# Optimization experiments

Measured on AMD Instinct MI355X. Metric: run time of the kernel, lower is better.

The kernel has to match this reference:

```python
import jax, jax.numpy as jnp
import numpy as np

B, T = 512, 512
NQ, K, M, DK, DV, DF = 1000, 5, 50, 64, 256, 50
ABILITY_SCALE = 3.0


def setup_inputs() -> dict:
    key = jax.random.key(0)
    ks = jax.random.split(key, 16)
    s = 0.05
    p = {}
    p["q_data"] = jax.random.randint(ks[0], (B, T), 0, NQ + 1)
    p["r_data"] = jax.random.randint(ks[1], (B, T), 0, K)
    p["q_embed_W"] = jax.random.normal(ks[2], (NQ + 1, DK)) * s
    p["Mk"] = jax.random.normal(ks[3], (M, DK)) * s
    p["Mv0"] = jax.random.normal(ks[4], (M, DV)) * s
    p["value_W"] = jax.random.normal(ks[5], (2 * NQ, DV)) * s
    p["value_b"] = jnp.zeros((DV,))
    p["erase_W"] = jax.random.normal(ks[6], (DV, DV)) * s
    p["erase_b"] = jnp.zeros((DV,))
    p["add_W"] = jax.random.normal(ks[7], (DV, DV)) * s
    p["add_b"] = jnp.zeros((DV,))
    p["summary_W"] = jax.random.normal(ks[8], (DV + DK, DF)) * s
    p["summary_b"] = jnp.zeros((DF,))
    p["ability_W"] = jax.random.normal(ks[9], (DF, 1)) * s
    p["ability_b"] = jnp.zeros((1,))
    p["thresh_W"] = jax.random.normal(ks[10], (DK, K - 1)) * s
    p["thresh_b"] = jnp.zeros((K - 1,))
    p["disc_W"] = jax.random.normal(ks[11], (DF + DK, 1)) * s
    p["disc_b"] = jnp.zeros((1,))
    p["corn_W"] = jax.random.normal(ks[12], (DF + DK, K - 1)) * s
    p["corn_b"] = jnp.zeros((K - 1,))
    return p


def reference(q_data, r_data, q_embed_W, Mk, Mv0, value_W, value_b, erase_W, erase_b,
              add_W, add_b, summary_W, summary_b, ability_W, ability_b,
              thresh_W, thresh_b, disc_W, disc_b, corn_W, corn_b):
    nq = value_W.shape[0] // 2
    k_cats = corn_W.shape[1] + 1
    b = q_data.shape[0]
    qe = q_embed_W[q_data]                                # [B,T,DK] question key embedding
    valid = (q_data > 0)[..., None]                       # q==0 is padding (one-hot col dropped)
    idx = jnp.maximum(q_data - 1, 0)
    # ordered embedding [one_hot(q), (r/(K-1))*one_hot(q)] @ value_W == exact row gather
    rs = r_data.astype(qe.dtype) / (k_cats - 1)
    ve = value_W[idx] + rs[..., None] * value_W[nq + idx]
    ve = jnp.where(valid, ve, 0.0) + value_b              # [B,T,DV]
    # attention over key memory (time-independent, hoisted out of the recurrence)
    w = jax.nn.softmax(jnp.einsum('btk,mk->btm', qe, Mk), axis=-1)  # [B,T,M]
    erase = jax.nn.sigmoid(ve @ erase_W + erase_b)        # [B,T,DV]
    add = jnp.tanh(ve @ add_W + add_b)                    # [B,T,DV]
    Mv_init = jnp.broadcast_to(Mv0, (b,) + Mv0.shape)     # [B,M,DV]

    def step(Mv, inp):
        w_t, e_t, a_t = inp                               # [B,M], [B,DV], [B,DV]
        read = jnp.einsum('bm,bmv->bv', w_t, Mv)          # read BEFORE write (t reads state < t)
        Mv = Mv * (1.0 - w_t[:, :, None] * e_t[:, None, :]) + w_t[:, :, None] * a_t[:, None, :]
        return Mv, read

    _, reads = jax.lax.scan(step, Mv_init,
                            (jnp.swapaxes(w, 0, 1), jnp.swapaxes(erase, 0, 1), jnp.swapaxes(add, 0, 1)))
    reads = jnp.swapaxes(reads, 0, 1)                     # [B,T,DV]

    summary = jnp.tanh(jnp.concatenate([reads, qe], -1) @ summary_W + summary_b)  # [B,T,DF]
    theta = (summary @ ability_W + ability_b)[..., 0] * ABILITY_SCALE             # [B,T]
    betas = qe @ thresh_W + thresh_b                                              # [B,T,K-1]
    di = jnp.concatenate([summary, qe], -1)                                       # [B,T,DF+DK]
    alpha = jax.nn.softplus(di @ disc_W + disc_b)[..., 0]                         # [B,T]
    logits = di @ corn_W + corn_b                                                 # [B,T,K-1]
    # CORN: cumulative conditional probs -> class probabilities
    cp = jnp.cumprod(jax.nn.sigmoid(logits), axis=-1)     # P(y > k)
    upper = jnp.concatenate([jnp.ones_like(cp[..., :1]), cp], -1)
    lower = jnp.concatenate([cp, jnp.zeros_like(cp[..., :1])], -1)
    probs = upper - lower                                 # [B,T,K]
    return theta, betas, alpha, probs, logits
```

## Files before the change

### kernel.cpp

```cpp
#include <hip/hip_runtime.h>

typedef unsigned short u16;
typedef unsigned int u32;
typedef __bf16 bf16x8 __attribute__((ext_vector_type(8)));
typedef float fx4 __attribute__((ext_vector_type(4)));
typedef float fx2 __attribute__((ext_vector_type(2)));

#define NT 262144
#define B_SZ 512
#define T_LEN 512
#define NQv 1000
#define LP 40
#define VE_ROWS 5120

__device__ __forceinline__ float bf2f(u16 u) { return __uint_as_float(((u32)u) << 16); }
__device__ __forceinline__ u16 f2bf(float f) {
    u32 x = __float_as_uint(f);
    x += 0x7fffu + ((x >> 16) & 1u);
    return (u16)(x >> 16);
}
__device__ __forceinline__ u32 pack2(float a, float b) {
    return (u32)f2bf(a) | ((u32)f2bf(b) << 16);
}
__device__ __forceinline__ float sigm(float x) { return 1.0f / (1.0f + __expf(-x)); }
__device__ __forceinline__ float tanh_fast(float x) {
    float e2 = __expf(2.0f * x);
    return 1.0f - 2.0f / (e2 + 1.0f);
}
__device__ __forceinline__ void load_lds16(const void* g, void* l) {
    __builtin_amdgcn_global_load_lds(
        (const __attribute__((address_space(1))) u32*)g,
        (__attribute__((address_space(3))) u32*)l, 16, 0, 0);
}

__global__ __launch_bounds__(256) void k_prep_w(const float* __restrict__ eW,
                                                const float* __restrict__ aW,
                                                const float* __restrict__ sW,
                                                u16* __restrict__ Wt,
                                                u16* __restrict__ SWt) {
    int id = blockIdx.x * 256 + threadIdx.x;
    if (id < 131072) {
        int n = id >> 8, k = id & 255;
        Wt[n * 256 + k] = f2bf((n < 256) ? eW[k * 256 + n] : aW[k * 256 + (n - 256)]);
    } else {
        int id2 = id - 131072;
        if (id2 < 64 * 320) {
            int n = id2 / 320, k = id2 - n * 320;
            SWt[n * 320 + k] = (n < 50) ? f2bf(sW[k * 50 + n]) : (u16)0;
        }
    }
}

__global__ __launch_bounds__(256) void k_w_tab(const float* __restrict__ qeW,
                                               const float* __restrict__ Mk,
                                               float* __restrict__ w_tab) {
    __shared__ __align__(16) float mk[3200];
    int tid = threadIdx.x;
    for (int i = tid; i < 3200; i += 256) mk[i] = Mk[i];
    int q = blockIdx.x * 256 + tid;
    __syncthreads();
    if (q > NQv) return;

    float qe[64];
    {
        const float4* qr = (const float4*)(qeW + (size_t)q * 64);
#pragma unroll
        for (int i = 0; i < 16; i++) {
            float4 u = qr[i];
            qe[4 * i + 0] = u.x; qe[4 * i + 1] = u.y;
            qe[4 * i + 2] = u.z; qe[4 * i + 3] = u.w;
        }
    }
    float lg[50];
#pragma unroll
    for (int m = 0; m < 50; m++) {
        const float* mr = &mk[m * 64];
        float acc = 0.f;
#pragma unroll
        for (int k = 0; k < 64; k++) acc = fmaf(qe[k], mr[k], acc);
        lg[m] = acc;
    }
    float mx = -1e30f;
#pragma unroll
    for (int m = 0; m < 50; m++) mx = fmaxf(mx, lg[m]);
    float sum = 0.f;
#pragma unroll
    for (int m = 0; m < 50; m++) { lg[m] = __expf(lg[m] - mx); sum += lg[m]; }
    float inv = 1.0f / sum;
#pragma unroll
    for (int m = 0; m < 50; m++) w_tab[(size_t)q * 50 + m] = lg[m] * inv;
}

__global__ __launch_bounds__(256) void k_ve_tab(const float* __restrict__ vW,
                                                const float* __restrict__ vb,
                                                u16* __restrict__ ve_tab) {
    int id = blockIdx.x * 256 + threadIdx.x;
    int row = id >> 5, seg = id & 31;
    if (row >= VE_ROWS) return;
    int q = row / 5;
    int r = row - q * 5;
    if (q > NQv) q = NQv;
    int idx = (q > 0) ? (q - 1) : 0;
    float rs = (float)r * 0.25f;
    float vf = (q > 0) ? 1.0f : 0.0f;

    const float* pa = vW + (size_t)idx * 256 + seg * 8;
    const float* pb = pa + NQv * 256;
    float4 a0 = ((const float4*)pa)[0];
    float4 a1 = ((const float4*)pa)[1];
    float4 b0 = ((const float4*)pb)[0];
    float4 b1 = ((const float4*)pb)[1];
    const float* vbp = vb + seg * 8;
    float o0 = vf * fmaf(rs, b0.x, a0.x) + vbp[0];
    float o1 = vf * fmaf(rs, b0.y, a0.y) + vbp[1];
    float o2 = vf * fmaf(rs, b0.z, a0.z) + vbp[2];
    float o3 = vf * fmaf(rs, b0.w, a0.w) + vbp[3];
    float o4 = vf * fmaf(rs, b1.x, a1.x) + vbp[4];
    float o5 = vf * fmaf(rs, b1.y, a1.y) + vbp[5];
    float o6 = vf * fmaf(rs, b1.z, a1.z) + vbp[6];
    float o7 = vf * fmaf(rs, b1.w, a1.w) + vbp[7];
    uint4 o;
    o.x = pack2(o0, o1); o.y = pack2(o2, o3);
    o.z = pack2(o4, o5); o.w = pack2(o6, o7);
    *(uint4*)(ve_tab + (size_t)row * 256 + seg * 8) = o;
}

__global__ __launch_bounds__(256) void k_gemm_ea(const u16* __restrict__ ve,
                                                 const u16* __restrict__ Wt,
                                                 const float* __restrict__ eb,
                                                 const float* __restrict__ ab,
                                                 u16* __restrict__ e_out,
                                                 u16* __restrict__ a_out) {
    __shared__ __align__(16) u16 smem[8192];
    u16* lA = smem;
    u16* lB = smem + 4096;

    int tid = threadIdx.x;
    int row0 = blockIdx.x * 128;
    int col0 = blockIdx.y * 128;

    int wave = tid >> 6, lane = tid & 63;
    int wm = wave >> 1, wn = wave & 1;
    int rl = lane & 15, quad = lane >> 4;
    fx4 acc[4][4] = {};

    int c0 = tid, c1 = tid + 256;
    int r0_ = c0 >> 2, j0 = c0 & 3;
    int r1_ = c1 >> 2, j1 = c1 & 3;

    for (int k0 = 0; k0 < 256; k0 += 32) {
        load_lds16(ve + (size_t)(row0 + r0_) * 256 + k0 + j0 * 8, lA + c0 * 8);
        load_lds16(ve + (size_t)(row0 + r1_) * 256 + k0 + j1 * 8, lA + c1 * 8);
        load_lds16(Wt + (size_t)(col0 + r0_) * 256 + k0 + j0 * 8, lB + c0 * 8);
        load_lds16(Wt + (size_t)(col0 + r1_) * 256 + k0 + j1 * 8, lB + c1 * 8);
        __syncthreads();
        bf16x8 af[4], bfr[4];
#pragma unroll
        for (int i = 0; i < 4; i++) af[i] = *(const bf16x8*)(lA + (wm * 64 + i * 16 + rl) * 32 + quad * 8);
#pragma unroll
        for (int j = 0; j < 4; j++) bfr[j] = *(const bf16x8*)(lB + (wn * 64 + j * 16 + rl) * 32 + quad * 8);
#pragma unroll
        for (int i = 0; i < 4; i++)
#pragma unroll
            for (int j = 0; j < 4; j++)
                acc[i][j] = __builtin_amdgcn_mfma_f32_16x16x32_bf16(af[i], bfr[j], acc[i][j], 0, 0, 0);
        __syncthreads();
    }

    bool is_er = (col0 < 256);
    const float* bias = is_er ? eb : ab;
    u16* outp = is_er ? e_out : a_out;
    int cb0 = col0 & 255;
    u16* cst = smem;
#pragma unroll
    for (int h = 0; h < 2; h++) {
        if (wm == h) {
#pragma unroll
            for (int j = 0; j < 4; j++) {
                int nl = wn * 64 + j * 16 + rl;
                float bv = bias[cb0 + nl];
#pragma unroll
                for (int i = 0; i < 4; i++) {
                    int rowl = i * 16 + quad * 4;
#pragma unroll
                    for (int r = 0; r < 4; r++) {
                        float x = acc[i][j][r] + bv;
                        cst[(rowl + r) * 128 + nl] = f2bf(is_er ? sigm(x) : tanh_fast(x));
                    }
                }
            }
        }
        __syncthreads();
#pragma unroll
        for (int c = 0; c < 4; c++) {
            int idx = c * 256 + tid;
            int row = idx >> 4, seg = idx & 15;
            *(uint4*)(outp + (size_t)(row0 + h * 64 + row) * 256 + cb0 + seg * 8) =
                *(const uint4*)(cst + row * 128 + seg * 8);
        }
        __syncthreads();
    }
}

__global__ __launch_bounds__(256) void k_scan(const int* __restrict__ q_data,
                                              const int* __restrict__ r_data,
                                              const float* __restrict__ w_tab,
                                              const u16* __restrict__ e_tab,
                                              const u16* __restrict__ a_tab,
                                              const float* __restrict__ Mv0,
                                              u16* __restrict__ reads_out) {
    int b = blockIdx.x;
    int tid = threadIdx.x;
    __shared__ float wls[2][8][52];

    const int* qp = q_data + (size_t)b * T_LEN;
    const int* rp = r_data + (size_t)b * T_LEN;

    fx2 Mv[25];
#pragma unroll
    for (int i = 0; i < 25; i++) {
        Mv[i].x = Mv0[(2 * i) * 256 + tid];
        Mv[i].y = Mv0[(2 * i + 1) * 256 + tid];
    }

    u16 eu[8], au[8];
#pragma unroll
    for (int s = 0; s < 8; s++) {
        int qr = qp[s] * 5 + rp[s];
        eu[s] = e_tab[(size_t)qr * 256 + tid];
        au[s] = a_tab[(size_t)qr * 256 + tid];
    }
    if (tid < 200) {
        int s = tid / 25, m2 = tid % 25;
        float2 w0 = ((const float2*)(w_tab + (size_t)qp[s] * 50))[m2];
        wls[0][s][2 * m2] = w0.x;
        wls[0][s][2 * m2 + 1] = w0.y;
    }
    __syncthreads();

    const int ngrp = T_LEN / 8;
    for (int g = 0; g < ngrp; g++) {
        int cur = g & 1, nxt = cur ^ 1;
        bool has_next = (g + 1 < ngrp);
        int tn0 = (g + 1) * 8;

        u16 eun[8], aun[8];
        float2 wn_ = make_float2(0.f, 0.f);
        if (has_next) {
#pragma unroll
            for (int s = 0; s < 8; s++) {
                int qr = qp[tn0 + s] * 5 + rp[tn0 + s];
                eun[s] = e_tab[(size_t)qr * 256 + tid];
                aun[s] = a_tab[(size_t)qr * 256 + tid];
            }
            if (tid < 200) {
                int s = tid / 25, m2 = tid % 25;
                wn_ = ((const float2*)(w_tab + (size_t)qp[tn0 + s] * 50))[m2];
            }
        }

#pragma unroll
        for (int s = 0; s < 8; s++) {
            float e = bf2f(eu[s]), a = bf2f(au[s]);
            fx2 e2; e2.x = e; e2.y = e;
            fx2 a2; a2.x = a; a2.y = a;
            const fx2* wv = (const fx2*)&wls[cur][s][0];
            fx2 rd2; rd2.x = 0.f; rd2.y = 0.f;
#pragma unroll
            for (int i = 0; i < 25; i++) {
                fx2 w2 = wv[i];
                rd2 = rd2 + w2 * Mv[i];
                fx2 t2 = a2 - e2 * Mv[i];
                Mv[i] = Mv[i] + w2 * t2;
            }
            float rd = rd2.x + rd2.y;
            reads_out[((size_t)b * T_LEN + g * 8 + s) * 256 + tid] = f2bf(rd);
        }

        if (has_next) {
            if (tid < 200) {
                int s = tid / 25, m2 = tid % 25;
                wls[nxt][s][2 * m2] = wn_.x;
                wls[nxt][s][2 * m2 + 1] = wn_.y;
            }
#pragma unroll
            for (int s = 0; s < 8; s++) { eu[s] = eun[s]; au[s] = aun[s]; }
        }
        __syncthreads();
    }
}

__global__ __launch_bounds__(256) void k_sum_heads(const u16* __restrict__ reads,
                                                   const int* __restrict__ q_data,
                                                   const float* __restrict__ qeW,
                                                   const u16* __restrict__ SWt,
                                                   const float* __restrict__ sb,
                                                   const float* __restrict__ abilW,
                                                   const float* __restrict__ abilb,
                                                   const float* __restrict__ tW,
                                                   const float* __restrict__ tb,
                                                   const float* __restrict__ dW,
                                                   const float* __restrict__ db,
                                                   const float* __restrict__ cW,
                                                   const float* __restrict__ cb,
                                                   float* __restrict__ out,
                                                   int t0, int tcl2) {
    __shared__ __align__(16) u16 lA[128 * LP];
    __shared__ __align__(16) u16 lB[64 * LP];
    __shared__ float sS[128 * 52];
    __shared__ int s_q[128];
    int tid = threadIdx.x;
    int row0 = blockIdx.x * 128;
    if (tid < 128) {
        int ctok = row0 + tid;
        int b = ctok >> tcl2;
        int tc = ctok & ((1 << tcl2) - 1);
        s_q[tid] = q_data[(b << 9) + t0 + tc];
    }
    int wave = tid >> 6, lane = tid & 63;
    int wm = wave >> 1, wn = wave & 1;
    int rl = lane & 15, quad = lane >> 4;
    fx4 acc[4][2] = {};
    __syncthreads();

    for (int ks = 0; ks < 10; ks++) {
        int k0 = ks * 32;
#pragma unroll
        for (int h = 0; h < 2; h++) {
            int c = tid + h * 256;
            int row = c >> 2, j = c & 3;
            if (k0 < 256) {
                uint4 u = *(const uint4*)(reads + (size_t)(row0 + row) * 256 + k0 + j * 8);
                *(uint4*)(lA + row * LP + j * 8) = u;
            } else {
                const float* src = qeW + (size_t)s_q[row] * 64 + (k0 - 256) + j * 8;
                float4 f0 = ((const float4*)src)[0];
                float4 f1 = ((const float4*)src)[1];
                uint4 o;
                o.x = pack2(f0.x, f0.y); o.y = pack2(f0.z, f0.w);
                o.z = pack2(f1.x, f1.y); o.w = pack2(f1.z, f1.w);
                *(uint4*)(lA + row * LP + j * 8) = o;
            }
        }
        {
            int n = tid >> 2, j = tid & 3;
            uint4 u = *(const uint4*)(SWt + (size_t)n * 320 + k0 + j * 8);
            *(uint4*)(lB + n * LP + j * 8) = u;
        }
        __syncthreads();
        bf16x8 af[4], bfr[2];
#pragma unroll
        for (int i = 0; i < 4; i++) af[i] = *(const bf16x8*)(lA + (wm * 64 + i * 16 + rl) * LP + quad * 8);
#pragma unroll
        for (int j = 0; j < 2; j++) bfr[j] = *(const bf16x8*)(lB + (wn * 32 + j * 16 + rl) * LP + quad * 8);
#pragma unroll
        for (int i = 0; i < 4; i++)
#pragma unroll
            for (int j = 0; j < 2; j++)
                acc[i][j] = __builtin_amdgcn_mfma_f32_16x16x32_bf16(af[i], bfr[j], acc[i][j], 0, 0, 0);
        __syncthreads();
    }

#pragma unroll
    for (int j = 0; j < 2; j++) {
        int n = wn * 32 + j * 16 + rl;
        if (n < 50) {
            float bv = sb[n];
#pragma unroll
            for (int i = 0; i < 4; i++) {
                int rowl = wm * 64 + i * 16 + quad * 4;
#pragma unroll
                for (int r = 0; r < 4; r++)
                    sS[(rowl + r) * 52 + n] = tanh_fast(acc[i][j][r] + bv);
            }
        }
    }
    __syncthreads();

    if (tid < 128) {
        int ctok = row0 + tid;
        int b = ctok >> tcl2;
        int tc = ctok & ((1 << tcl2) - 1);
        int gtok = (b << 9) + t0 + tc;
        const float* sp = &sS[tid * 52];

        float qe[64];
        const float4* qr = (const float4*)(qeW + (size_t)s_q[tid] * 64);
#pragma unroll
        for (int i = 0; i < 16; i++) {
            float4 u = qr[i];
            qe[4 * i + 0] = u.x; qe[4 * i + 1] = u.y;
            qe[4 * i + 2] = u.z; qe[4 * i + 3] = u.w;
        }
        float th = abilb[0];
#pragma unroll
        for (int j = 0; j < 50; j++) th = fmaf(sp[j], abilW[j], th);
        out[gtok] = th * 3.0f;

        float bt0 = tb[0], bt1 = tb[1], bt2 = tb[2], bt3 = tb[3];
#pragma unroll
        for (int k = 0; k < 64; k++) {
            float x = qe[k];
            bt0 = fmaf(x, tW[k * 4 + 0], bt0);
            bt1 = fmaf(x, tW[k * 4 + 1], bt1);
            bt2 = fmaf(x, tW[k * 4 + 2], bt2);
            bt3 = fmaf(x, tW[k * 4 + 3], bt3);
        }
        out[NT + (size_t)gtok * 4 + 0] = bt0;
        out[NT + (size_t)gtok * 4 + 1] = bt1;
        out[NT + (size_t)gtok * 4 + 2] = bt2;
        out[NT + (size_t)gtok * 4 + 3] = bt3;

        float da = db[0];
        float l0 = cb[0], l1 = cb[1], l2 = cb[2], l3 = cb[3];
#pragma unroll
        for (int i = 0; i < 50; i++) {
            float x = sp[i];
            da = fmaf(x, dW[i], da);
            l0 = fmaf(x, cW[i * 4 + 0], l0);
            l1 = fmaf(x, cW[i * 4 + 1], l1);
            l2 = fmaf(x, cW[i * 4 + 2], l2);
            l3 = fmaf(x, cW[i * 4 + 3], l3);
        }
#pragma unroll
        for (int k = 0; k < 64; k++) {
            float x = qe[k];
            int i = 50 + k;
            da = fmaf(x, dW[i], da);
            l0 = fmaf(x, cW[i * 4 + 0], l0);
            l1 = fmaf(x, cW[i * 4 + 1], l1);
            l2 = fmaf(x, cW[i * 4 + 2], l2);
            l3 = fmaf(x, cW[i * 4 + 3], l3);
        }
        float alpha = logf(1.0f + __expf(da));
        out[5 * (size_t)NT + gtok] = alpha;

        out[11 * (size_t)NT + (size_t)gtok * 4 + 0] = l0;
        out[11 * (size_t)NT + (size_t)gtok * 4 + 1] = l1;
        out[11 * (size_t)NT + (size_t)gtok * 4 + 2] = l2;
        out[11 * (size_t)NT + (size_t)gtok * 4 + 3] = l3;

        float c0 = sigm(l0);
        float c1 = c0 * sigm(l1);
        float c2 = c1 * sigm(l2);
        float c3 = c2 * sigm(l3);
        size_t pb = 6 * (size_t)NT + (size_t)gtok * 5;
        out[pb + 0] = 1.0f - c0;
        out[pb + 1] = c0 - c1;
        out[pb + 2] = c1 - c2;
        out[pb + 3] = c2 - c3;
        out[pb + 4] = c3;
    }
}

extern "C" void kernel_launch(void* const* d_in, const int* in_sizes, int n_in,
                              void* d_out, int out_size, void* d_ws, size_t ws_size,
                              hipStream_t stream) {
    (void)in_sizes; (void)n_in; (void)out_size; (void)ws_size;
    const int* q_data = (const int*)d_in[0];
    const int* r_data = (const int*)d_in[1];
    const float* qeW = (const float*)d_in[2];
    const float* Mk  = (const float*)d_in[3];
    const float* Mv0 = (const float*)d_in[4];
    const float* vW  = (const float*)d_in[5];
    const float* vb  = (const float*)d_in[6];
    const float* eW  = (const float*)d_in[7];
    const float* eb  = (const float*)d_in[8];
    const float* aW  = (const float*)d_in[9];
    const float* ab  = (const float*)d_in[10];
    const float* sW  = (const float*)d_in[11];
    const float* sb  = (const float*)d_in[12];
    const float* abilW = (const float*)d_in[13];
    const float* abilb = (const float*)d_in[14];
    const float* tW  = (const float*)d_in[15];
    const float* tb  = (const float*)d_in[16];
    const float* dW  = (const float*)d_in[17];
    const float* db  = (const float*)d_in[18];
    const float* cW  = (const float*)d_in[19];
    const float* cb  = (const float*)d_in[20];

    char* ws = (char*)d_ws;
    u16* Wt     = (u16*)(ws + 0);
    u16* SWt    = (u16*)(ws + 262144);
    float* w_tab = (float*)(ws + 303104);
    u16* ve_tab = (u16*)(ws + 507904);
    u16* e_tab  = (u16*)(ws + 3129344);
    u16* a_tab  = (u16*)(ws + 5750784);
    u16* reads  = (u16*)(ws + 8372224);
    float* out = (float*)d_out;

    k_prep_w<<<592, 256, 0, stream>>>(eW, aW, sW, Wt, SWt);
    k_w_tab<<<4, 256, 0, stream>>>(qeW, Mk, w_tab);
    k_ve_tab<<<VE_ROWS / 8, 256, 0, stream>>>(vW, vb, ve_tab);
    dim3 g2(VE_ROWS / 128, 4);
    k_gemm_ea<<<g2, 256, 0, stream>>>(ve_tab, Wt, eb, ab, e_tab, a_tab);
    k_scan<<<B_SZ, 256, 0, stream>>>(q_data, r_data, w_tab, e_tab, a_tab, Mv0, reads);
    k_sum_heads<<<NT / 128, 256, 0, stream>>>(reads, q_data, qeW, SWt, sb,
                                              abilW, abilb, tW, tb, dW, db, cW, cb,
                                              out, 0, 9);
}
```

Before: 457.5 us.

## Fuse summary GEMM and heads into scan kernel, precompute per-question tables

The scan kernel now keeps each 128-token block of reads in LDS and, every 16 groups, runs the summary MFMA GEMM over the read part plus the per-token heads inline, so the reads buffer is never written to or read back from global memory. The question-embedding contributions (summary qe part, betas, disc and corn qe parts) are precomputed into per-question tables by a new small kernel and then gathered per token. This removes the separate k_sum_heads launch and the reads round trip. In exchange the scan kernel uses much more LDS (about 66 KB), which may cut occupancy, and the serial scan now stalls periodically for the GEMM and head work.

```diff
diff --git a/kernel.cpp b/kernel.cpp
--- a/kernel.cpp
+++ b/kernel.cpp
@@ -10,8 +10,9 @@
 #define B_SZ 512
 #define T_LEN 512
 #define NQv 1000
-#define LP 40
 #define VE_ROWS 5120
+#define TLP 264
+#define SSP 53
 
 __device__ __forceinline__ float bf2f(u16 u) { return __uint_as_float(((u32)u) << 16); }
 __device__ __forceinline__ u16 f2bf(float f) {
@@ -44,9 +45,9 @@
         Wt[n * 256 + k] = f2bf((n < 256) ? eW[k * 256 + n] : aW[k * 256 + (n - 256)]);
     } else {
         int id2 = id - 131072;
-        if (id2 < 64 * 320) {
-            int n = id2 / 320, k = id2 - n * 320;
-            SWt[n * 320 + k] = (n < 50) ? f2bf(sW[k * 50 + n]) : (u16)0;
+        if (id2 < 16384) {
+            int n = id2 >> 8, k = id2 & 255;
+            SWt[n * 256 + k] = (n < 50) ? f2bf(sW[k * 50 + n]) : (u16)0;
         }
     }
 }
@@ -125,6 +126,52 @@
     *(uint4*)(ve_tab + (size_t)row * 256 + seg * 8) = o;
 }
 
+__global__ __launch_bounds__(256) void k_q_tabs(const float* __restrict__ qeW,
+                                                const float* __restrict__ sW,
+                                                const float* __restrict__ tW,
+                                                const float* __restrict__ tb,
+                                                const float* __restrict__ dW,
+                                                const float* __restrict__ cW,
+                                                float* __restrict__ sq_tab,
+                                                float* __restrict__ beta_tab,
+                                                float* __restrict__ dq_tab,
+                                                float* __restrict__ cq_tab) {
+    int id = blockIdx.x * 256 + threadIdx.x;
+    int q = id >> 6, n = id & 63;
+    if (q > NQv) return;
+    float qe[64];
+    const float4* qr = (const float4*)(qeW + (size_t)q * 64);
+#pragma unroll
+    for (int i = 0; i < 16; i++) {
+        float4 u = qr[i];
+        qe[4 * i + 0] = u.x; qe[4 * i + 1] = u.y;
+        qe[4 * i + 2] = u.z; qe[4 * i + 3] = u.w;
+    }
+    if (n < 50) {
+        float acc = 0.f;
+#pragma unroll
+        for (int k = 0; k < 64; k++) acc = fmaf(qe[k], sW[(256 + k) * 50 + n], acc);
+        sq_tab[(size_t)q * 50 + n] = acc;
+    } else if (n < 54) {
+        int j = n - 50;
+        float acc = tb[j];
+#pragma unroll
+        for (int k = 0; k < 64; k++) acc = fmaf(qe[k], tW[k * 4 + j], acc);
+        beta_tab[(size_t)q * 4 + j] = acc;
+    } else if (n == 54) {
+        float acc = 0.f;
+#pragma unroll
+        for (int k = 0; k < 64; k++) acc = fmaf(qe[k], dW[50 + k], acc);
+        dq_tab[q] = acc;
+    } else if (n >= 56 && n < 60) {
+        int j = n - 56;
+        float acc = 0.f;
+#pragma unroll
+        for (int k = 0; k < 64; k++) acc = fmaf(qe[k], cW[(50 + k) * 4 + j], acc);
+        cq_tab[(size_t)q * 4 + j] = acc;
+    }
+}
+
 __global__ __launch_bounds__(256) void k_gemm_ea(const u16* __restrict__ ve,
                                                  const u16* __restrict__ Wt,
                                                  const float* __restrict__ eb,
@@ -202,19 +249,37 @@
     }
 }
 
-__global__ __launch_bounds__(256) void k_scan(const int* __restrict__ q_data,
-                                              const int* __restrict__ r_data,
-                                              const float* __restrict__ w_tab,
-                                              const u16* __restrict__ e_tab,
-                                              const u16* __restrict__ a_tab,
-                                              const float* __restrict__ Mv0,
-                                              u16* __restrict__ reads_out) {
+__global__ __launch_bounds__(256) void k_fused(const int* __restrict__ q_data,
+                                               const int* __restrict__ r_data,
+                                               const float* __restrict__ w_tab,
+                                               const u16* __restrict__ e_tab,
+                                               const u16* __restrict__ a_tab,
+                                               const float* __restrict__ Mv0,
+                                               const u16* __restrict__ SWt,
+                                               const float* __restrict__ sq_tab,
+                                               const float* __restrict__ sb,
+                                               const float* __restrict__ abilW,
+                                               const float* __restrict__ abilb,
+                                               const float* __restrict__ beta_tab,
+                                               const float* __restrict__ dW,
+                                               const float* __restrict__ db,
+                                               const float* __restrict__ dq_tab,
+                                               const float* __restrict__ cW,
+                                               const float* __restrict__ cb,
+                                               const float* __restrict__ cq_tab,
+                                               float* __restrict__ out) {
     int b = blockIdx.x;
     int tid = threadIdx.x;
+    __shared__ __align__(16) u16 tileA[128 * TLP];
     __shared__ float wls[2][8][52];
+    __shared__ int sq_idx[128];
 
     const int* qp = q_data + (size_t)b * T_LEN;
     const int* rp = r_data + (size_t)b * T_LEN;
+
+    int wave = tid >> 6, lane = tid & 63;
+    int wm = wave >> 1, wn = wave & 1;
+    int rl = lane & 15, quad = lane >> 4;
 
     fx2 Mv[25];
 #pragma unroll
@@ -273,8 +338,8 @@
                 fx2 t2 = a2 - e2 * Mv[i];
                 Mv[i] = Mv[i] + w2 * t2;
             }
-            float rd = rd2.x + rd2.y;
-            reads_out[((size_t)b * T_LEN + g * 8 + s) * 256 + tid] = f2bf(rd);
+            int tokrow = (g * 8 + s) & 127;
+            tileA[tokrow * TLP + tid] = f2bf(rd2.x + rd2.y);
         }
 
         if (has_next) {
@@ -287,169 +352,98 @@
             for (int s = 0; s < 8; s++) { eu[s] = eun[s]; au[s] = aun[s]; }
         }
         __syncthreads();
-    }
-}
-
-__global__ __launch_bounds__(256) void k_sum_heads(const u16* __restrict__ reads,
-                                                   const int* __restrict__ q_data,
-                                                   const float* __restrict__ qeW,
-                                                   const u16* __restrict__ SWt,
-                                                   const float* __restrict__ sb,
-                                                   const float* __restrict__ abilW,
-                                                   const float* __restrict__ abilb,
-                                                   const float* __restrict__ tW,
-                                                   const float* __restrict__ tb,
-                                                   const float* __restrict__ dW,
-                                                   const float* __restrict__ db,
-                                                   const float* __restrict__ cW,
-                                                   const float* __restrict__ cb,
-                                                   float* __restrict__ out,
-                                                   int t0, int tcl2) {
-    __shared__ __align__(16) u16 lA[128 * LP];
-    __shared__ __align__(16) u16 lB[64 * LP];
-    __shared__ float sS[128 * 52];
-    __shared__ int s_q[128];
-    int tid = threadIdx.x;
-    int row0 = blockIdx.x * 128;
-    if (tid < 128) {
-        int ctok = row0 + tid;
-        int b = ctok >> tcl2;
-        int tc = ctok & ((1 << tcl2) - 1);
-        s_q[tid] = q_data[(b << 9) + t0 + tc];
-    }
-    int wave = tid >> 6, lane = tid & 63;
-    int wm = wave >> 1, wn = wave & 1;
-    int rl = lane & 15, quad = lane >> 4;
-    fx4 acc[4][2] = {};
-    __syncthreads();
-
-    for (int ks = 0; ks < 10; ks++) {
-        int k0 = ks * 32;
-#pragma unroll
-        for (int h = 0; h < 2; h++) {
-            int c = tid + h * 256;
-            int row = c >> 2, j = c & 3;
-            if (k0 < 256) {
-                uint4 u = *(const uint4*)(reads + (size_t)(row0 + row) * 256 + k0 + j * 8);
-                *(uint4*)(lA + row * LP + j * 8) = u;
-            } else {
-                const float* src = qeW + (size_t)s_q[row] * 64 + (k0 - 256) + j * 8;
-                float4 f0 = ((const float4*)src)[0];
-                float4 f1 = ((const float4*)src)[1];
-                uint4 o;
-                o.x = pack2(f0.x, f0.y); o.y = pack2(f0.z, f0.w);
-                o.z = pack2(f1.x, f1.y); o.w = pack2(f1.z, f1.w);
-                *(uint4*)(lA + row * LP + j * 8) = o;
-            }
-        }
-        {
-            int n = tid >> 2, j = tid & 3;
-            uint4 u = *(const uint4*)(SWt + (size_t)n * 320 + k0 + j * 8);
-            *(uint4*)(lB + n * LP + j * 8) = u;
-        }
-        __syncthreads();
-        bf16x8 af[4], bfr[2];
-#pragma unroll
-        for (int i = 0; i < 4; i++) af[i] = *(const bf16x8*)(lA + (wm * 64 + i * 16 + rl) * LP + quad * 8);
-#pragma unroll
-        for (int j = 0; j < 2; j++) bfr[j] = *(const bf16x8*)(lB + (wn * 32 + j * 16 + rl) * LP + quad * 8);
-#pragma unroll
-        for (int i = 0; i < 4; i++)
-#pragma unroll
-            for (int j = 0; j < 2; j++)
-                acc[i][j] = __builtin_amdgcn_mfma_f32_16x16x32_bf16(af[i], bfr[j], acc[i][j], 0, 0, 0);
-        __syncthreads();
-    }
-
-#pragma unroll
-    for (int j = 0; j < 2; j++) {
-        int n = wn * 32 + j * 16 + rl;
-        if (n < 50) {
-            float bv = sb[n];
-#pragma unroll
-            for (int i = 0; i < 4; i++) {
-                int rowl = wm * 64 + i * 16 + quad * 4;
-#pragma unroll
-                for (int r = 0; r < 4; r++)
-                    sS[(rowl + r) * 52 + n] = tanh_fast(acc[i][j][r] + bv);
-            }
-        }
-    }
-    __syncthreads();
-
-    if (tid < 128) {
-        int ctok = row0 + tid;
-        int b = ctok >> tcl2;
-        int tc = ctok & ((1 << tcl2) - 1);
-        int gtok = (b << 9) + t0 + tc;
-        const float* sp = &sS[tid * 52];
-
-        float qe[64];
-        const float4* qr = (const float4*)(qeW + (size_t)s_q[tid] * 64);
-#pragma unroll
-        for (int i = 0; i < 16; i++) {
-            float4 u = qr[i];
-            qe[4 * i + 0] = u.x; qe[4 * i + 1] = u.y;
-            qe[4 * i + 2] = u.z; qe[4 * i + 3] = u.w;
-        }
-        float th = abilb[0];
-#pragma unroll
-        for (int j = 0; j < 50; j++) th = fmaf(sp[j], abilW[j], th);
-        out[gtok] = th * 3.0f;
-
-        float bt0 = tb[0], bt1 = tb[1], bt2 = tb[2], bt3 = tb[3];
-#pragma unroll
-        for (int k = 0; k < 64; k++) {
-            float x = qe[k];
-            bt0 = fmaf(x, tW[k * 4 + 0], bt0);
-            bt1 = fmaf(x, tW[k * 4 + 1], bt1);
-            bt2 = fmaf(x, tW[k * 4 + 2], bt2);
-            bt3 = fmaf(x, tW[k * 4 + 3], bt3);
-        }
-        out[NT + (size_t)gtok * 4 + 0] = bt0;
-        out[NT + (size_t)gtok * 4 + 1] = bt1;
-        out[NT + (size_t)gtok * 4 + 2] = bt2;
-        out[NT + (size_t)gtok * 4 + 3] = bt3;
-
-        float da = db[0];
-        float l0 = cb[0], l1 = cb[1], l2 = cb[2], l3 = cb[3];
-#pragma unroll
-        for (int i = 0; i < 50; i++) {
-            float x = sp[i];
-            da = fmaf(x, dW[i], da);
-            l0 = fmaf(x, cW[i * 4 + 0], l0);
-            l1 = fmaf(x, cW[i * 4 + 1], l1);
-            l2 = fmaf(x, cW[i * 4 + 2], l2);
-            l3 = fmaf(x, cW[i * 4 + 3], l3);
-        }
-#pragma unroll
-        for (int k = 0; k < 64; k++) {
-            float x = qe[k];
-            int i = 50 + k;
-            da = fmaf(x, dW[i], da);
-            l0 = fmaf(x, cW[i * 4 + 0], l0);
-            l1 = fmaf(x, cW[i * 4 + 1], l1);
-            l2 = fmaf(x, cW[i * 4 + 2], l2);
-            l3 = fmaf(x, cW[i * 4 + 3], l3);
-        }
-        float alpha = logf(1.0f + __expf(da));
-        out[5 * (size_t)NT + gtok] = alpha;
-
-        out[11 * (size_t)NT + (size_t)gtok * 4 + 0] = l0;
-        out[11 * (size_t)NT + (size_t)gtok * 4 + 1] = l1;
-        out[11 * (size_t)NT + (size_t)gtok * 4 + 2] = l2;
-        out[11 * (size_t)NT + (size_t)gtok * 4 + 3] = l3;
-
-        float c0 = sigm(l0);
-        float c1 = c0 * sigm(l1);
-        float c2 = c1 * sigm(l2);
-        float c3 = c2 * sigm(l3);
-        size_t pb = 6 * (size_t)NT + (size_t)gtok * 5;
-        out[pb + 0] = 1.0f - c0;
-        out[pb + 1] = c0 - c1;
-        out[pb + 2] = c1 - c2;
-        out[pb + 3] = c2 - c3;
-        out[pb + 4] = c3;
+
+        if ((g & 15) == 15) {
+            int tile0 = (g >> 4) * 128;
+            if (tid < 128) sq_idx[tid] = qp[tile0 + tid];
+
+            fx4 acc[4][2] = {};
+#pragma unroll
+            for (int ks = 0; ks < 8; ks++) {
+                int k0 = ks * 32;
+                bf16x8 af[4], bfr[2];
+#pragma unroll
+                for (int i = 0; i < 4; i++)
+                    af[i] = *(const bf16x8*)(tileA + (wm * 64 + i * 16 + rl) * TLP + k0 + quad * 8);
+#pragma unroll
+                for (int j = 0; j < 2; j++)
+                    bfr[j] = *(const bf16x8*)(SWt + (size_t)(wn * 32 + j * 16 + rl) * 256 + k0 + quad * 8);
+#pragma unroll
+                for (int i = 0; i < 4; i++)
+#pragma unroll
+                    for (int j = 0; j < 2; j++)
+                        acc[i][j] = __builtin_amdgcn_mfma_f32_16x16x32_bf16(af[i], bfr[j], acc[i][j], 0, 0, 0);
+            }
+            __syncthreads();
+
+            float* sS = (float*)tileA;
+#pragma unroll
+            for (int j = 0; j < 2; j++) {
+                int n = wn * 32 + j * 16 + rl;
+                if (n < 50) {
+#pragma unroll
+                    for (int i = 0; i < 4; i++) {
+                        int rowl = wm * 64 + i * 16 + quad * 4;
+#pragma unroll
+                        for (int r = 0; r < 4; r++)
+                            sS[(rowl + r) * SSP + n] = acc[i][j][r];
+                    }
+                }
+            }
+            __syncthreads();
+
+            if (tid < 128) {
+                int q = sq_idx[tid];
+                size_t gtok = (size_t)b * T_LEN + tile0 + tid;
+                const float* sq = sq_tab + (size_t)q * 50;
+                const float* sp = sS + tid * SSP;
+
+                float th = abilb[0];
+                float da = db[0];
+                float l0 = cb[0], l1 = cb[1], l2 = cb[2], l3 = cb[3];
+#pragma unroll
+                for (int i = 0; i < 50; i++) {
+                    float sv = tanh_fast(sp[i] + sq[i] + sb[i]);
+                    th = fmaf(sv, abilW[i], th);
+                    da = fmaf(sv, dW[i], da);
+                    l0 = fmaf(sv, cW[i * 4 + 0], l0);
+                    l1 = fmaf(sv, cW[i * 4 + 1], l1);
+                    l2 = fmaf(sv, cW[i * 4 + 2], l2);
+                    l3 = fmaf(sv, cW[i * 4 + 3], l3);
+                }
+                da += dq_tab[q];
+                l0 += cq_tab[q * 4 + 0];
+                l1 += cq_tab[q * 4 + 1];
+                l2 += cq_tab[q * 4 + 2];
+                l3 += cq_tab[q * 4 + 3];
+
+                out[gtok] = th * 3.0f;
+
+                out[NT + gtok * 4 + 0] = beta_tab[q * 4 + 0];
+                out[NT + gtok * 4 + 1] = beta_tab[q * 4 + 1];
+                out[NT + gtok * 4 + 2] = beta_tab[q * 4 + 2];
+                out[NT + gtok * 4 + 3] = beta_tab[q * 4 + 3];
+
+                out[5 * (size_t)NT + gtok] = logf(1.0f + __expf(da));
+
+                out[11 * (size_t)NT + gtok * 4 + 0] = l0;
+                out[11 * (size_t)NT + gtok * 4 + 1] = l1;
+                out[11 * (size_t)NT + gtok * 4 + 2] = l2;
+                out[11 * (size_t)NT + gtok * 4 + 3] = l3;
+
+                float c0 = sigm(l0);
+                float c1 = c0 * sigm(l1);
+                float c2 = c1 * sigm(l2);
+                float c3 = c2 * sigm(l3);
+                size_t pb = 6 * (size_t)NT + gtok * 5;
+                out[pb + 0] = 1.0f - c0;
+                out[pb + 1] = c0 - c1;
+                out[pb + 2] = c1 - c2;
+                out[pb + 3] = c2 - c3;
+                out[pb + 4] = c3;
+            }
+            __syncthreads();
+        }
     }
 }
 
@@ -480,22 +474,26 @@
     const float* cb  = (const float*)d_in[20];
 
     char* ws = (char*)d_ws;
-    u16* Wt     = (u16*)(ws + 0);
-    u16* SWt    = (u16*)(ws + 262144);
-    float* w_tab = (float*)(ws + 303104);
-    u16* ve_tab = (u16*)(ws + 507904);
-    u16* e_tab  = (u16*)(ws + 3129344);
-    u16* a_tab  = (u16*)(ws + 5750784);
-    u16* reads  = (u16*)(ws + 8372224);
+    u16* Wt        = (u16*)(ws + 0);
+    u16* SWt       = (u16*)(ws + 262144);
+    float* w_tab   = (float*)(ws + 327680);
+    float* sq_tab  = (float*)(ws + 532480);
+    float* beta_tab= (float*)(ws + 737280);
+    float* dq_tab  = (float*)(ws + 753664);
+    float* cq_tab  = (float*)(ws + 757760);
+    u16* ve_tab    = (u16*)(ws + 774144);
+    u16* e_tab     = (u16*)(ws + 3395584);
+    u16* a_tab     = (u16*)(ws + 6017024);
     float* out = (float*)d_out;
 
-    k_prep_w<<<592, 256, 0, stream>>>(eW, aW, sW, Wt, SWt);
+    k_prep_w<<<576, 256, 0, stream>>>(eW, aW, sW, Wt, SWt);
     k_w_tab<<<4, 256, 0, stream>>>(qeW, Mk, w_tab);
     k_ve_tab<<<VE_ROWS / 8, 256, 0, stream>>>(vW, vb, ve_tab);
+    k_q_tabs<<<256, 256, 0, stream>>>(qeW, sW, tW, tb, dW, cW,
+                                      sq_tab, beta_tab, dq_tab, cq_tab);
     dim3 g2(VE_ROWS / 128, 4);
     k_gemm_ea<<<g2, 256, 0, stream>>>(ve_tab, Wt, eb, ab, e_tab, a_tab);
-    k_scan<<<B_SZ, 256, 0, stream>>>(q_data, r_data, w_tab, e_tab, a_tab, Mv0, reads);
-    k_sum_heads<<<NT / 128, 256, 0, stream>>>(reads, q_data, qeW, SWt, sb,
-                                              abilW, abilb, tW, tb, dW, db, cW, cb,
-                                              out, 0, 9);
-}
+    k_fused<<<B_SZ, 256, 0, stream>>>(q_data, r_data, w_tab, e_tab, a_tab, Mv0,
+                                      SWt, sq_tab, sb, abilW, abilb, beta_tab,
+                                      dW, db, dq_tab, cW, cb, cq_tab, out);
+}
```

New measurement: 464.7 us. About the same (+1.6%).
